# Performance work log

Measured on AMD Instinct MI355X. Metric: run time of the kernel, lower is better.

Reference implementation:

```python
import jax, jax.numpy as jnp
import numpy as np

N_NODES = 50000


def _gcn_conv(h, src, dst, W, b):
    # h: [N, d_in] -> [N, d_out]; symmetric-normalized aggregation with self-loops
    N = h.shape[0]
    h = h @ W  # transform first (d_out < d_in), like PyG GCNConv
    deg = jax.ops.segment_sum(jnp.ones_like(dst, dtype=h.dtype), dst, num_segments=N)
    dinv = jnp.where(deg > 0, jax.lax.rsqrt(jnp.maximum(deg, 1.0)), 0.0)
    norm = dinv[src] * dinv[dst]  # [E']
    msg = h[src] * norm[:, None]  # [E', d_out]
    out = jax.ops.segment_sum(msg, dst, num_segments=N)
    return out + b


def setup_inputs() -> dict:
    key = jax.random.key(0)
    k1, k2, k3, k4 = jax.random.split(key, 4)
    dim_in, dim_h, dim_out, E = 512, 96, 40, 800000
    x = jax.random.normal(k1, (N_NODES, dim_in), dtype=jnp.float32)
    edge_index = jax.random.randint(k2, (2, E), 0, N_NODES, dtype=jnp.int64)
    W1 = jax.random.normal(k3, (dim_in, dim_h), dtype=jnp.float32) / np.sqrt(dim_in)
    b1 = jnp.zeros((dim_h,), dtype=jnp.float32)
    W2 = jax.random.normal(k4, (dim_h, dim_out), dtype=jnp.float32) / np.sqrt(dim_h)
    b2 = jnp.zeros((dim_out,), dtype=jnp.float32)
    return {"x": x, "edge_index": edge_index, "W1": W1, "b1": b1, "W2": W2, "b2": b2}


def reference(x, edge_index, W1, b1, W2, b2):
    N = x.shape[0]
    loops = jnp.arange(N, dtype=edge_index.dtype)
    src = jnp.concatenate([edge_index[0], loops])
    dst = jnp.concatenate([edge_index[1], loops])
    h = jax.nn.relu(_gcn_conv(x, src, dst, W1, b1))
    # dropout p=0.5 is identity in eval mode (training=False)
    logits = _gcn_conv(h, src, dst, W2, b2)
    return (logits, jax.nn.log_softmax(logits, axis=1))
```

## Files before the change

### kernel.cpp

```cpp
#include <hip/hip_runtime.h>
#include <hip/hip_bf16.h>
#include <cstdint>
#include <cstddef>

#define DIN 512
#define DH  96
#define DOUT 40

typedef __attribute__((ext_vector_type(8))) short s8v;
typedef __attribute__((ext_vector_type(4))) float f4v;

__device__ __forceinline__ ushort f2bf(float f) {
    uint u = __float_as_uint(f);
    u += 0x7fffu + ((u >> 16) & 1u);
    return (ushort)(u >> 16);
}
__device__ __forceinline__ uint f2bf2(float lo, float hi) {
    __hip_bfloat162 h = __float22bfloat162_rn(make_float2(lo, hi));
    return *(uint*)&h;
}
__device__ __forceinline__ float bflo(uint u) { return __uint_as_float(u << 16); }
__device__ __forceinline__ float bfhi(uint u) { return __uint_as_float(u & 0xffff0000u); }

__global__ __launch_bounds__(256) void k_prep(
    const float* __restrict__ W1, const float* __restrict__ W2,
    int* __restrict__ cnt, ushort* __restrict__ W1T, ushort* __restrict__ W2T, int N)
{
    int i = blockIdx.x * 256 + threadIdx.x;
    if (i < N) cnt[i] = 0;
    if (i < DIN * DH) {
        int k = i / DH, n = i % DH;
        W1T[(size_t)n * DIN + k] = f2bf(W1[i]);
    }
    if (i < 48 * DH) {
        int n = i / DH, k = i % DH;
        W2T[i] = (n < DOUT) ? f2bf(W2[(size_t)k * DOUT + n]) : (ushort)0;
    }
}

__global__ __launch_bounds__(256) void k_hist(
    const int* __restrict__ dst, int* __restrict__ cnt, int* __restrict__ pos, int E)
{
    int e = blockIdx.x * 256 + threadIdx.x;
    if (e < E) pos[e] = atomicAdd(&cnt[dst[e]], 1);
}

__global__ __launch_bounds__(256) void k_blocksum(const int* __restrict__ cnt, int* __restrict__ bsum, int N) {
    int i = blockIdx.x * 256 + threadIdx.x;
    int c = (i < N) ? cnt[i] : 0;
    #pragma unroll
    for (int off = 32; off >= 1; off >>= 1) c += __shfl_down(c, off, 64);
    __shared__ int wsum[4];
    if ((threadIdx.x & 63) == 0) wsum[threadIdx.x >> 6] = c;
    __syncthreads();
    if (threadIdx.x == 0) bsum[blockIdx.x] = wsum[0] + wsum[1] + wsum[2] + wsum[3];
}

__global__ __launch_bounds__(256) void k_scan_small(const int* __restrict__ bsum, int* __restrict__ boff, int SB) {
    __shared__ int p[256];
    int tid = threadIdx.x;
    int v = (tid < SB) ? bsum[tid] : 0;
    p[tid] = v;
    __syncthreads();
    #pragma unroll
    for (int off = 1; off < 256; off <<= 1) {
        int t = (tid >= off) ? p[tid - off] : 0;
        __syncthreads();
        p[tid] += t;
        __syncthreads();
    }
    if (tid < SB) boff[tid] = p[tid] - v;
}

__global__ __launch_bounds__(256) void k_rowptr(
    const int* __restrict__ cnt, const int* __restrict__ boff,
    int* __restrict__ row_ptr, float* __restrict__ dinv, int N)
{
    __shared__ int p[256];
    int tid = threadIdx.x;
    int i = blockIdx.x * 256 + tid;
    int c = (i < N) ? cnt[i] : 0;
    p[tid] = c;
    __syncthreads();
    #pragma unroll
    for (int off = 1; off < 256; off <<= 1) {
        int t = (tid >= off) ? p[tid - off] : 0;
        __syncthreads();
        p[tid] += t;
        __syncthreads();
    }
    int excl = p[tid] - c;
    if (i < N) {
        int base = boff[blockIdx.x] + excl;
        row_ptr[i] = base;
        dinv[i] = rsqrtf(1.0f + (float)c);
        if (i == N - 1) row_ptr[N] = base + c;
    }
}

__global__ __launch_bounds__(256) void k_fill(
    const int* __restrict__ src, const int* __restrict__ dst,
    const int* __restrict__ row_ptr, const int* __restrict__ pos,
    int* __restrict__ adj, int E)
{
    int e = blockIdx.x * 256 + threadIdx.x;
    if (e >= E) return;
    adj[row_ptr[dst[e]] + pos[e]] = src[e];
}

#define SWZ(r) (((r >> 1) & 3) << 3)
__global__ __launch_bounds__(256) void k_gemm1(
    const float* __restrict__ x, const ushort* __restrict__ W1T,
    const float* __restrict__ dinv, ushort* __restrict__ hs1, int N)
{
    __shared__ __align__(16) ushort lds[14336];
    const int tid = threadIdx.x;
    const int row0 = blockIdx.x * 128;
    const int lane = tid & 63, w = tid >> 6;
    const int rb = (w >> 1) * 64, cb = (w & 1) * 48;
    const int lm = lane & 15, lq = lane >> 4;

    int aof[4], bof[3];
    #pragma unroll
    for (int i = 0; i < 4; ++i) {
        int r = rb + i * 16 + lm;
        aof[i] = r * 32 + ((lq * 8) ^ SWZ(r));
    }
    #pragma unroll
    for (int j = 0; j < 3; ++j) {
        int n = cb + j * 16 + lm;
        bof[j] = 8192 + n * 32 + ((lq * 8) ^ SWZ(n));
    }

    f4v acc[4][3];
    #pragma unroll
    for (int i = 0; i < 4; ++i)
        #pragma unroll
        for (int j = 0; j < 3; ++j) acc[i][j] = (f4v)0.f;

    const int sr = tid >> 1;
    const int c0 = (tid & 1) * 16;

    auto stage = [&](int kt, int buf) {
        int k0 = kt * 32;
        int gr = row0 + sr;
        ushort* A = lds + buf * 4096;
        #pragma unroll
        for (int s = 0; s < 2; ++s) {
            int c = c0 + s * 8;
            float4 v0 = make_float4(0.f, 0.f, 0.f, 0.f), v1 = v0;
            if (gr < N) {
                const float* pp = &x[(size_t)gr * DIN + k0 + c];
                v0 = *(const float4*)pp;
                v1 = *(const float4*)(pp + 4);
            }
            uint4 wv;
            wv.x = f2bf2(v0.x, v0.y);
            wv.y = f2bf2(v0.z, v0.w);
            wv.z = f2bf2(v1.x, v1.y);
            wv.w = f2bf2(v1.z, v1.w);
            *(uint4*)&A[sr * 32 + (c ^ SWZ(sr))] = wv;
        }
        ushort* B = lds + 8192 + buf * 3072;
        #pragma unroll
        for (int f = tid; f < 384; f += 256) {
            int n = f >> 2, c = (f & 3) * 8;
            uint4 wv = *(const uint4*)&W1T[(size_t)n * DIN + k0 + c];
            *(uint4*)&B[n * 32 + (c ^ SWZ(n))] = wv;
        }
    };

    stage(0, 0);
    for (int kt = 0; kt < 16; ++kt) {
        __syncthreads();
        if (kt < 15) stage(kt + 1, (kt + 1) & 1);
        const int ab = (kt & 1) * 4096;
        const int bb = (kt & 1) * 3072;
        s8v b0 = *(s8v*)&lds[bof[0] + bb];
        s8v b1 = *(s8v*)&lds[bof[1] + bb];
        s8v b2 = *(s8v*)&lds[bof[2] + bb];
        #pragma unroll
        for (int i = 0; i < 4; ++i) {
            s8v a = *(s8v*)&lds[aof[i] + ab];
            acc[i][0] = __builtin_amdgcn_mfma_f32_16x16x32_bf16(a, b0, acc[i][0], 0, 0, 0);
            acc[i][1] = __builtin_amdgcn_mfma_f32_16x16x32_bf16(a, b1, acc[i][1], 0, 0, 0);
            acc[i][2] = __builtin_amdgcn_mfma_f32_16x16x32_bf16(a, b2, acc[i][2], 0, 0, 0);
        }
    }

    #pragma unroll
    for (int i = 0; i < 4; ++i) {
        int gr0 = row0 + rb + i * 16 + lq * 4;
        #pragma unroll
        for (int q = 0; q < 4; ++q) {
            int gr = gr0 + q;
            if (gr < N) {
                float di = dinv[gr];
                #pragma unroll
                for (int j = 0; j < 3; ++j)
                    hs1[(size_t)gr * DH + cb + j * 16 + lm] = f2bf(acc[i][j][q] * di);
            }
        }
    }
}

__global__ __launch_bounds__(256) void k_agg1(
    const int* __restrict__ row_ptr, const int* __restrict__ adj,
    const float* __restrict__ dinv, const ushort* __restrict__ hs1,
    const float* __restrict__ b1, ushort* __restrict__ h1, int N)
{
    int t = blockIdx.x * 256 + threadIdx.x;
    int node = t >> 6, lane = t & 63;
    if (node >= N) return;
    int c = lane << 1;
    const bool act = (c < DH);

    float a0 = 0.f, a1 = 0.f;
    if (act) {
        uint u = *(const uint*)&hs1[(size_t)node * DH + c];
        a0 = bflo(u); a1 = bfhi(u);
    }
    int e = row_ptr[node], e1 = row_ptr[node + 1];
    for (; e + 7 < e1; e += 8) {
        int s0 = adj[e],     s1 = adj[e + 1], s2 = adj[e + 2], s3 = adj[e + 3];
        int s4 = adj[e + 4], s5 = adj[e + 5], s6 = adj[e + 6], s7 = adj[e + 7];
        if (act) {
            uint u0 = *(const uint*)&hs1[(size_t)s0 * DH + c];
            uint u1 = *(const uint*)&hs1[(size_t)s1 * DH + c];
            uint u2 = *(const uint*)&hs1[(size_t)s2 * DH + c];
            uint u3 = *(const uint*)&hs1[(size_t)s3 * DH + c];
            uint u4 = *(const uint*)&hs1[(size_t)s4 * DH + c];
            uint u5 = *(const uint*)&hs1[(size_t)s5 * DH + c];
            uint u6 = *(const uint*)&hs1[(size_t)s6 * DH + c];
            uint u7 = *(const uint*)&hs1[(size_t)s7 * DH + c];
            a0 += bflo(u0); a1 += bfhi(u0);
            a0 += bflo(u1); a1 += bfhi(u1);
            a0 += bflo(u2); a1 += bfhi(u2);
            a0 += bflo(u3); a1 += bfhi(u3);
            a0 += bflo(u4); a1 += bfhi(u4);
            a0 += bflo(u5); a1 += bfhi(u5);
            a0 += bflo(u6); a1 += bfhi(u6);
            a0 += bflo(u7); a1 += bfhi(u7);
        }
    }
    for (; e < e1; ++e) {
        int s = adj[e];
        if (act) {
            uint u = *(const uint*)&hs1[(size_t)s * DH + c];
            a0 += bflo(u); a1 += bfhi(u);
        }
    }
    if (act) {
        float di = dinv[node];
        float r0 = fmaxf(fmaf(a0, di, b1[c]), 0.f);
        float r1 = fmaxf(fmaf(a1, di, b1[c + 1]), 0.f);
        *(uint*)&h1[(size_t)node * DH + c] = f2bf2(r0, r1);
    }
}

__global__ __launch_bounds__(256) void k_gemm2(
    const ushort* __restrict__ h1, const ushort* __restrict__ W2T,
    const float* __restrict__ dinv, ushort* __restrict__ hs2b, int N)
{
    __shared__ __align__(16) ushort lds[16384 + 48 * 128];
    const int tid = threadIdx.x;
    const int row0 = blockIdx.x * 128;

    for (int f = tid; f < 576; f += 256) {
        int r = f / 12, c = (f % 12) * 8;
        uint4 v = *(const uint4*)&W2T[r * DH + c];
        *(uint4*)&lds[16384 + r * 128 + (c ^ ((r & 7) << 3))] = v;
    }
    {
        int r = tid >> 1, half = tid & 1;
        int gr = row0 + r;
        #pragma unroll
        for (int i = 0; i < 6; ++i) {
            int c = half * 48 + i * 8;
            uint4 v = make_uint4(0, 0, 0, 0);
            if (gr < N) v = *(const uint4*)&h1[(size_t)gr * DH + c];
            *(uint4*)&lds[r * 128 + (c ^ ((r & 7) << 3))] = v;
        }
    }
    __syncthreads();

    const int lane = tid & 63, w = tid >> 6;
    const int rb = w * 32, lm = lane & 15, lq = lane >> 4;
    f4v acc[2][3];
    #pragma unroll
    for (int i = 0; i < 2; ++i)
        #pragma unroll
        for (int j = 0; j < 3; ++j) acc[i][j] = (f4v)0.f;

    #pragma unroll
    for (int ks = 0; ks < 3; ++ks) {
        int kk = ks * 32 + lq * 8;
        s8v b[3];
        #pragma unroll
        for (int j = 0; j < 3; ++j) {
            int n = j * 16 + lm;
            b[j] = *(s8v*)&lds[16384 + n * 128 + (kk ^ ((n & 7) << 3))];
        }
        #pragma unroll
        for (int i = 0; i < 2; ++i) {
            int r = rb + i * 16 + lm;
            s8v a = *(s8v*)&lds[r * 128 + (kk ^ ((r & 7) << 3))];
            #pragma unroll
            for (int j = 0; j < 3; ++j)
                acc[i][j] = __builtin_amdgcn_mfma_f32_16x16x32_bf16(a, b[j], acc[i][j], 0, 0, 0);
        }
    }

    #pragma unroll
    for (int i = 0; i < 2; ++i) {
        int gr0 = row0 + rb + i * 16 + lq * 4;
        #pragma unroll
        for (int q = 0; q < 4; ++q) {
            int gr = gr0 + q;
            if (gr < N) {
                float di = dinv[gr];
                #pragma unroll
                for (int j = 0; j < 3; ++j) {
                    int col = j * 16 + lm;
                    if (col < DOUT)
                        hs2b[(size_t)gr * 64 + col] = f2bf(acc[i][j][q] * di);
                }
            }
        }
    }
}

__global__ __launch_bounds__(256) void k_agg2sm(
    const int* __restrict__ row_ptr, const int* __restrict__ adj,
    const float* __restrict__ dinv, const ushort* __restrict__ hs2b,
    const float* __restrict__ b2, float* __restrict__ out,
    float* __restrict__ lsm, int N)
{
    int t = blockIdx.x * 256 + threadIdx.x;
    int node = t >> 6, lane = t & 63;
    if (node >= N) return;
    int c = lane << 1;
    const bool act = (c < DOUT);

    float a0 = 0.f, a1 = 0.f;
    if (act) {
        uint u = *(const uint*)&hs2b[(size_t)node * 64 + c];
        a0 = bflo(u); a1 = bfhi(u);
    }
    int e = row_ptr[node], e1 = row_ptr[node + 1];
    for (; e + 7 < e1; e += 8) {
        int s0 = adj[e],     s1 = adj[e + 1], s2 = adj[e + 2], s3 = adj[e + 3];
        int s4 = adj[e + 4], s5 = adj[e + 5], s6 = adj[e + 6], s7 = adj[e + 7];
        if (act) {
            uint u0 = *(const uint*)&hs2b[(size_t)s0 * 64 + c];
            uint u1 = *(const uint*)&hs2b[(size_t)s1 * 64 + c];
            uint u2 = *(const uint*)&hs2b[(size_t)s2 * 64 + c];
            uint u3 = *(const uint*)&hs2b[(size_t)s3 * 64 + c];
            uint u4 = *(const uint*)&hs2b[(size_t)s4 * 64 + c];
            uint u5 = *(const uint*)&hs2b[(size_t)s5 * 64 + c];
            uint u6 = *(const uint*)&hs2b[(size_t)s6 * 64 + c];
            uint u7 = *(const uint*)&hs2b[(size_t)s7 * 64 + c];
            a0 += bflo(u0); a1 += bfhi(u0);
            a0 += bflo(u1); a1 += bfhi(u1);
            a0 += bflo(u2); a1 += bfhi(u2);
            a0 += bflo(u3); a1 += bfhi(u3);
            a0 += bflo(u4); a1 += bfhi(u4);
            a0 += bflo(u5); a1 += bfhi(u5);
            a0 += bflo(u6); a1 += bfhi(u6);
            a0 += bflo(u7); a1 += bfhi(u7);
        }
    }
    for (; e < e1; ++e) {
        int s = adj[e];
        if (act) {
            uint u = *(const uint*)&hs2b[(size_t)s * 64 + c];
            a0 += bflo(u); a1 += bfhi(u);
        }
    }

    float di = act ? dinv[node] : 0.f;
    float v0 = act ? fmaf(a0, di, b2[c]) : -1e30f;
    float v1 = act ? fmaf(a1, di, b2[c + 1]) : -1e30f;
    float m = fmaxf(v0, v1);
    #pragma unroll
    for (int off = 32; off >= 1; off >>= 1) m = fmaxf(m, __shfl_xor(m, off));
    float ex = act ? (__expf(v0 - m) + __expf(v1 - m)) : 0.f;
    float s = ex;
    #pragma unroll
    for (int off = 32; off >= 1; off >>= 1) s += __shfl_xor(s, off);
    float lse = m + __logf(s);
    if (act) {
        *(float2*)&out[(size_t)node * DOUT + c] = make_float2(v0, v1);
        *(float2*)&lsm[(size_t)node * DOUT + c] = make_float2(v0 - lse, v1 - lse);
    }
}

extern "C" void kernel_launch(void* const* d_in, const int* in_sizes, int n_in,
                              void* d_out, int out_size, void* d_ws, size_t ws_size,
                              hipStream_t stream) {
    const float* x  = (const float*)d_in[0];
    const int*   ei = (const int*)d_in[1];
    const float* W1 = (const float*)d_in[2];
    const float* b1 = (const float*)d_in[3];
    const float* W2 = (const float*)d_in[4];
    const float* b2 = (const float*)d_in[5];

    const int N = in_sizes[0] / DIN;
    const int E = in_sizes[1] / 2;
    const int* srcp = ei;
    const int* dstp = ei + E;
    const int SB = (N + 255) / 256;

    ushort* hs1  = (ushort*)d_ws;
    ushort* h1   = hs1 + (size_t)N * DH;
    ushort* hs2b = h1 + (size_t)N * DH;
    float* dinv  = (float*)(hs2b + (size_t)N * 64);
    ushort* W1T  = (ushort*)(dinv + N);
    ushort* W2T  = W1T + (size_t)DH * DIN;
    int* cnt     = (int*)(W2T + 48 * DH);
    int* row_ptr = cnt + N;
    int* adj     = row_ptr + N + 1;
    int* pos     = adj + E;
    int* bsum    = pos + E;
    int* boff    = bsum + SB;

    float* out = (float*)d_out;
    float* lsm = out + (size_t)N * DOUT;

    const int gE = (E + 255) / 256;

    k_prep<<<SB, 256, 0, stream>>>(W1, W2, cnt, W1T, W2T, N);
    k_hist<<<gE, 256, 0, stream>>>(dstp, cnt, pos, E);
    k_blocksum<<<SB, 256, 0, stream>>>(cnt, bsum, N);
    k_scan_small<<<1, 256, 0, stream>>>(bsum, boff, SB);
    k_rowptr<<<SB, 256, 0, stream>>>(cnt, boff, row_ptr, dinv, N);
    k_fill<<<gE, 256, 0, stream>>>(srcp, dstp, row_ptr, pos, adj, E);

    k_gemm1<<<(N + 127) / 128, 256, 0, stream>>>(x, W1T, dinv, hs1, N);
    k_agg1<<<(int)(((size_t)N * 64 + 255) / 256), 256, 0, stream>>>(row_ptr, adj, dinv, hs1, b1, h1, N);

    k_gemm2<<<(N + 127) / 128, 256, 0, stream>>>(h1, W2T, dinv, hs2b, N);
    k_agg2sm<<<(int)(((size_t)N * 64 + 255) / 256), 256, 0, stream>>>(row_ptr, adj, dinv, hs2b, b2, out, lsm, N);
}
```

Before: 181.3 us.

## Fuse CSR prefix-scan kernels into one and halve GEMM1 row tile

Replaces the three-kernel scan (blocksum, small scan, rowptr) with a single kernel in which each block redundantly sums all preceding counts to get its base offset, removing two launches and their serialization. This trades launch overhead for quadratic redundant reads of cnt, about 196 blocks each reading up to 50K ints. Separately, GEMM1 tiles shrink from 128 to 64 rows per block, doubling the grid to 782 blocks for better CU occupancy on a 256-CU part. The cost is that the W1 tile is reloaded twice as often.

```diff
diff --git a/kernel.cpp b/kernel.cpp
--- a/kernel.cpp
+++ b/kernel.cpp
@@ -45,22 +45,26 @@
     if (e < E) pos[e] = atomicAdd(&cnt[dst[e]], 1);
 }
 
-__global__ __launch_bounds__(256) void k_blocksum(const int* __restrict__ cnt, int* __restrict__ bsum, int N) {
-    int i = blockIdx.x * 256 + threadIdx.x;
+__global__ __launch_bounds__(256) void k_rowptr_all(
+    const int* __restrict__ cnt, int* __restrict__ row_ptr,
+    float* __restrict__ dinv, int N)
+{
+    __shared__ int p[256];
+    __shared__ int wred[4];
+    const int tid = threadIdx.x, b = blockIdx.x;
+
+    int pre = 0;
+    const int limit = b * 256;
+    for (int j = tid; j < limit; j += 256) pre += cnt[j];
+    #pragma unroll
+    for (int off = 32; off >= 1; off >>= 1) pre += __shfl_down(pre, off, 64);
+    if ((tid & 63) == 0) wred[tid >> 6] = pre;
+    __syncthreads();
+    const int base0 = wred[0] + wred[1] + wred[2] + wred[3];
+
+    int i = b * 256 + tid;
     int c = (i < N) ? cnt[i] : 0;
-    #pragma unroll
-    for (int off = 32; off >= 1; off >>= 1) c += __shfl_down(c, off, 64);
-    __shared__ int wsum[4];
-    if ((threadIdx.x & 63) == 0) wsum[threadIdx.x >> 6] = c;
-    __syncthreads();
-    if (threadIdx.x == 0) bsum[blockIdx.x] = wsum[0] + wsum[1] + wsum[2] + wsum[3];
-}
-
-__global__ __launch_bounds__(256) void k_scan_small(const int* __restrict__ bsum, int* __restrict__ boff, int SB) {
-    __shared__ int p[256];
-    int tid = threadIdx.x;
-    int v = (tid < SB) ? bsum[tid] : 0;
-    p[tid] = v;
+    p[tid] = c;
     __syncthreads();
     #pragma unroll
     for (int off = 1; off < 256; off <<= 1) {
@@ -69,29 +73,9 @@
         p[tid] += t;
         __syncthreads();
     }
-    if (tid < SB) boff[tid] = p[tid] - v;
-}
-
-__global__ __launch_bounds__(256) void k_rowptr(
-    const int* __restrict__ cnt, const int* __restrict__ boff,
-    int* __restrict__ row_ptr, float* __restrict__ dinv, int N)
-{
-    __shared__ int p[256];
-    int tid = threadIdx.x;
-    int i = blockIdx.x * 256 + tid;
-    int c = (i < N) ? cnt[i] : 0;
-    p[tid] = c;
-    __syncthreads();
-    #pragma unroll
-    for (int off = 1; off < 256; off <<= 1) {
-        int t = (tid >= off) ? p[tid - off] : 0;
-        __syncthreads();
-        p[tid] += t;
-        __syncthreads();
-    }
     int excl = p[tid] - c;
     if (i < N) {
-        int base = boff[blockIdx.x] + excl;
+        int base = base0 + excl;
         row_ptr[i] = base;
         dinv[i] = rsqrtf(1.0f + (float)c);
         if (i == N - 1) row_ptr[N] = base + c;
@@ -113,60 +97,56 @@
     const float* __restrict__ x, const ushort* __restrict__ W1T,
     const float* __restrict__ dinv, ushort* __restrict__ hs1, int N)
 {
-    __shared__ __align__(16) ushort lds[14336];
+    __shared__ __align__(16) ushort lds[10240];
     const int tid = threadIdx.x;
-    const int row0 = blockIdx.x * 128;
+    const int row0 = blockIdx.x * 64;
     const int lane = tid & 63, w = tid >> 6;
-    const int rb = (w >> 1) * 64, cb = (w & 1) * 48;
+    const int rb = (w >> 1) * 32, cb = (w & 1) * 48;
     const int lm = lane & 15, lq = lane >> 4;
 
-    int aof[4], bof[3];
-    #pragma unroll
-    for (int i = 0; i < 4; ++i) {
+    int aof[2], bof[3];
+    #pragma unroll
+    for (int i = 0; i < 2; ++i) {
         int r = rb + i * 16 + lm;
         aof[i] = r * 32 + ((lq * 8) ^ SWZ(r));
     }
     #pragma unroll
     for (int j = 0; j < 3; ++j) {
         int n = cb + j * 16 + lm;
-        bof[j] = 8192 + n * 32 + ((lq * 8) ^ SWZ(n));
-    }
-
-    f4v acc[4][3];
-    #pragma unroll
-    for (int i = 0; i < 4; ++i)
+        bof[j] = 4096 + n * 32 + ((lq * 8) ^ SWZ(n));
+    }
+
+    f4v acc[2][3];
+    #pragma unroll
+    for (int i = 0; i < 2; ++i)
         #pragma unroll
         for (int j = 0; j < 3; ++j) acc[i][j] = (f4v)0.f;
 
-    const int sr = tid >> 1;
-    const int c0 = (tid & 1) * 16;
+    const int sr = tid >> 2;
+    const int c0 = (tid & 3) * 8;
 
     auto stage = [&](int kt, int buf) {
         int k0 = kt * 32;
         int gr = row0 + sr;
-        ushort* A = lds + buf * 4096;
-        #pragma unroll
-        for (int s = 0; s < 2; ++s) {
-            int c = c0 + s * 8;
-            float4 v0 = make_float4(0.f, 0.f, 0.f, 0.f), v1 = v0;
-            if (gr < N) {
-                const float* pp = &x[(size_t)gr * DIN + k0 + c];
-                v0 = *(const float4*)pp;
-                v1 = *(const float4*)(pp + 4);
-            }
-            uint4 wv;
-            wv.x = f2bf2(v0.x, v0.y);
-            wv.y = f2bf2(v0.z, v0.w);
-            wv.z = f2bf2(v1.x, v1.y);
-            wv.w = f2bf2(v1.z, v1.w);
-            *(uint4*)&A[sr * 32 + (c ^ SWZ(sr))] = wv;
-        }
-        ushort* B = lds + 8192 + buf * 3072;
+        ushort* A = lds + buf * 2048;
+        float4 v0 = make_float4(0.f, 0.f, 0.f, 0.f), v1 = v0;
+        if (gr < N) {
+            const float* pp = &x[(size_t)gr * DIN + k0 + c0];
+            v0 = *(const float4*)pp;
+            v1 = *(const float4*)(pp + 4);
+        }
+        uint4 wv;
+        wv.x = f2bf2(v0.x, v0.y);
+        wv.y = f2bf2(v0.z, v0.w);
+        wv.z = f2bf2(v1.x, v1.y);
+        wv.w = f2bf2(v1.z, v1.w);
+        *(uint4*)&A[sr * 32 + (c0 ^ SWZ(sr))] = wv;
+        ushort* B = lds + 4096 + buf * 3072;
         #pragma unroll
         for (int f = tid; f < 384; f += 256) {
-            int n = f >> 2, c = (f & 3) * 8;
-            uint4 wv = *(const uint4*)&W1T[(size_t)n * DIN + k0 + c];
-            *(uint4*)&B[n * 32 + (c ^ SWZ(n))] = wv;
+            int n = f >> 2, cc = (f & 3) * 8;
+            uint4 bv = *(const uint4*)&W1T[(size_t)n * DIN + k0 + cc];
+            *(uint4*)&B[n * 32 + (cc ^ SWZ(n))] = bv;
         }
     };
 
@@ -174,13 +154,13 @@
     for (int kt = 0; kt < 16; ++kt) {
         __syncthreads();
         if (kt < 15) stage(kt + 1, (kt + 1) & 1);
-        const int ab = (kt & 1) * 4096;
+        const int ab = (kt & 1) * 2048;
         const int bb = (kt & 1) * 3072;
         s8v b0 = *(s8v*)&lds[bof[0] + bb];
         s8v b1 = *(s8v*)&lds[bof[1] + bb];
         s8v b2 = *(s8v*)&lds[bof[2] + bb];
         #pragma unroll
-        for (int i = 0; i < 4; ++i) {
+        for (int i = 0; i < 2; ++i) {
             s8v a = *(s8v*)&lds[aof[i] + ab];
             acc[i][0] = __builtin_amdgcn_mfma_f32_16x16x32_bf16(a, b0, acc[i][0], 0, 0, 0);
             acc[i][1] = __builtin_amdgcn_mfma_f32_16x16x32_bf16(a, b1, acc[i][1], 0, 0, 0);
@@ -189,7 +169,7 @@
     }
 
     #pragma unroll
-    for (int i = 0; i < 4; ++i) {
+    for (int i = 0; i < 2; ++i) {
         int gr0 = row0 + rb + i * 16 + lq * 4;
         #pragma unroll
         for (int q = 0; q < 4; ++q) {
@@ -421,8 +401,6 @@
     int* row_ptr = cnt + N;
     int* adj     = row_ptr + N + 1;
     int* pos     = adj + E;
-    int* bsum    = pos + E;
-    int* boff    = bsum + SB;
 
     float* out = (float*)d_out;
     float* lsm = out + (size_t)N * DOUT;
@@ -431,12 +409,10 @@
 
     k_prep<<<SB, 256, 0, stream>>>(W1, W2, cnt, W1T, W2T, N);
     k_hist<<<gE, 256, 0, stream>>>(dstp, cnt, pos, E);
-    k_blocksum<<<SB, 256, 0, stream>>>(cnt, bsum, N);
-    k_scan_small<<<1, 256, 0, stream>>>(bsum, boff, SB);
-    k_rowptr<<<SB, 256, 0, stream>>>(cnt, boff, row_ptr, dinv, N);
+    k_rowptr_all<<<SB, 256, 0, stream>>>(cnt, row_ptr, dinv, N);
     k_fill<<<gE, 256, 0, stream>>>(srcp, dstp, row_ptr, pos, adj, E);
 
-    k_gemm1<<<(N + 127) / 128, 256, 0, stream>>>(x, W1T, dinv, hs1, N);
+    k_gemm1<<<(N + 63) / 64, 256, 0, stream>>>(x, W1T, dinv, hs1, N);
     k_agg1<<<(int)(((size_t)N * 64 + 255) / 256), 256, 0, stream>>>(row_ptr, adj, dinv, hs1, b1, h1, N);
 
     k_gemm2<<<(N + 127) / 128, 256, 0, stream>>>(h1, W2T, dinv, hs2b, N);
```

Result: slower. 203.8 us (+12.4%).
